# Performance work log

Measured on AMD Instinct MI355X. Metric: run time of the kernel, lower is better.

## Reference

```python
import jax, jax.numpy as jnp
import numpy as np

B, N, T, D = 2, 4, 512, 1024
DK, H, E = 64, 8, 6
D_ATTN = 512
DV = D_ATTN // H            # 64
DKP = 2 * DK                # PoPE doubles key dim -> 128
HE = H * E                  # 48
R = max(DK // 4, 1)         # LoRA rank 16
DA = int(DK * 1.618)        # 103
CC = D_ATTN                 # concat dim 512
DPG = max(int(CC * 0.618), 1)  # 316
ND = N * D
ROUTE_TEMP = 1.0


def _sinkhorn(M, n_iters=6):
    M = jnp.exp(M)
    for _ in range(n_iters):
        M = M / jnp.sum(M, -1, keepdims=True)
        M = M / jnp.sum(M, -2, keepdims=True)
    return M


def _pope(x, phi):
    mu = jax.nn.softplus(x)
    return jnp.concatenate([mu * jnp.cos(phi), mu * jnp.sin(phi)], -1)


def setup_inputs():
    ks = iter(jax.random.split(jax.random.key(0), 24))
    def rn(s, sc=0.01):
        return jax.random.normal(next(ks), s, jnp.float32) * sc
    return {
        'stream': jax.random.normal(next(ks), (B, N, T, D), jnp.float32),
        'freqs': 10000.0 ** (jnp.arange(DK, dtype=jnp.float32) / DK),
        'pope_delta_raw': jnp.zeros((DK,), jnp.float32),
        'W_q_w': rn((H, DK, D)), 'W_k_w': rn((H, DK, D)), 'W_v_w': rn((H, DV, D)),
        'q_router_w': rn((H, E, D), 0.02), 'kv_router_w': rn((H, E, D), 0.02),
        'lora_A_q': rn((HE, D, R)), 'lora_B_q': jnp.zeros((HE, R, DK), jnp.float32),
        'lora_A_k': rn((HE, D, R)), 'lora_B_k': jnp.zeros((HE, R, DK), jnp.float32),
        'lora_A_v': rn((HE, D, R)), 'lora_B_v': jnp.zeros((HE, R, DV), jnp.float32),
        'alpha_up_w': rn((HE, D, DA)), 'alpha_down_w': rn((HE, DA, DKP)),
        'beta_up_w': rn((HE, D, DA)), 'beta_down_w': rn((HE, DA, 1)),
        'mhc_norm_w': jnp.ones((HE, ND), jnp.float32),
        'phi_pre_w': rn((HE, N, ND)), 'phi_post_w': rn((HE, N, ND)),
        'phi_res_w': rn((HE, N * N, ND)),
        'b_pre': jnp.zeros((HE, N), jnp.float32), 'b_post': jnp.zeros((HE, N), jnp.float32),
        'b_res': jnp.zeros((HE, N, N), jnp.float32),
        'alpha_pre': jnp.ones((HE,), jnp.float32), 'alpha_post': jnp.ones((HE,), jnp.float32),
        'alpha_res': jnp.ones((HE,), jnp.float32),
        'batched_norm_w': jnp.ones((HE, D), jnp.float32),
        'W_pre_w': rn((HE, D, CC)), 'W_o_w': rn((D, CC)),
        'W_pg1_w': rn((HE, D, DPG)), 'W_pg2_w': rn((HE, DPG, D)),
    }


def reference(stream, freqs, pope_delta_raw, W_q_w, W_k_w, W_v_w, q_router_w, kv_router_w,
              lora_A_q, lora_B_q, lora_A_k, lora_B_k, lora_A_v, lora_B_v,
              alpha_up_w, alpha_down_w, beta_up_w, beta_down_w,
              mhc_norm_w, phi_pre_w, phi_post_w, phi_res_w, b_pre, b_post, b_res,
              alpha_pre, alpha_post, alpha_res, batched_norm_w,
              W_pre_w, W_o_w, W_pg1_w, W_pg2_w):
    positions = jnp.arange(T, dtype=jnp.float32)
    # ---- per-head top-1 routing (eval-mode argmax, straight-through probs) ----
    route_in = jnp.mean(stream, axis=1)                                # (B,T,D)
    q_logits = jnp.clip(jnp.einsum('btd,hed->hbte', route_in, q_router_w), -10, 10)
    kv_logits = jnp.clip(jnp.einsum('btd,hed->hbte', route_in, kv_router_w), -10, 10)
    q_probs = jax.nn.softmax(q_logits / ROUTE_TEMP, -1)
    kv_probs = jax.nn.softmax(kv_logits / ROUTE_TEMP, -1)
    q_oh = jax.nn.one_hot(jnp.argmax(q_logits, -1), E, dtype=stream.dtype)
    kv_oh = jax.nn.one_hot(jnp.argmax(kv_logits, -1), E, dtype=stream.dtype)
    eff_q = q_probs + jax.lax.stop_gradient(q_oh - q_probs)            # (H,B,T,E)
    eff_kv = kv_probs + jax.lax.stop_gradient(kv_oh - kv_probs)
    eff_q = eff_q.transpose(0, 3, 1, 2).reshape(HE, B, T)              # h-major, k=h*E+e
    eff_kv = eff_kv.transpose(0, 3, 1, 2).reshape(HE, B, T)
    # ---- batched MHC over all HE experts (dense form of active-set gather) ----
    x = stream.transpose(0, 2, 1, 3).reshape(B, T, ND)
    x = x * jax.lax.rsqrt(jnp.mean(jnp.square(x), -1, keepdims=True) + 1e-8)
    H_pre = jax.nn.sigmoid(alpha_pre[:, None, None, None] *
                           jnp.einsum('btd,knd->kbtn', x, phi_pre_w * mhc_norm_w[:, None, :])
                           + b_pre[:, None, None, :])
    H_post = 2 * jax.nn.sigmoid(alpha_post[:, None, None, None] *
                                jnp.einsum('btd,knd->kbtn', x, phi_post_w * mhc_norm_w[:, None, :])
                                + b_post[:, None, None, :])
    res = jnp.einsum('btd,knd->kbtn', x, phi_res_w * mhc_norm_w[:, None, :]).reshape(HE, B, T, N, N)
    H_res = _sinkhorn(alpha_res[:, None, None, None, None] * res + b_res[:, None, None, :, :])
    h_e = jnp.einsum('kbtn,bntd->kbtd', H_pre, stream)                 # (HE,B,T,D)
    h_e = h_e * jax.lax.rsqrt(jnp.mean(jnp.square(h_e), -1, keepdims=True) + 1e-8) * batched_norm_w[:, None, None, :]
    # ---- expert q/k/v with LoRA + PoPE ----
    phi = positions[:, None] * freqs[None, :]                          # (T,DK)
    phi_k = phi - 2 * jnp.pi * jax.nn.sigmoid(pope_delta_raw)[None, :]
    Wq = jnp.repeat(W_q_w, E, 0); Wk = jnp.repeat(W_k_w, E, 0); Wv = jnp.repeat(W_v_w, E, 0)
    def lora(h, A, Bm):
        return jnp.einsum('kbtr,kro->kbto', jax.nn.silu(jnp.einsum('kbtd,kdr->kbtr', h, A)), Bm)
    def l2n(v):
        return v * jax.lax.rsqrt(jnp.sum(jnp.square(v), -1, keepdims=True) + 1e-12)
    q_p = l2n(jnp.einsum('kbtd,kod->kbto', h_e, Wq) + lora(h_e, lora_A_q, lora_B_q))
    k_p = l2n(jnp.einsum('kbtd,kod->kbto', h_e, Wk) + lora(h_e, lora_A_k, lora_B_k))
    v_p = jnp.einsum('kbtd,kod->kbto', h_e, Wv) + lora(h_e, lora_A_v, lora_B_v)
    qmask = (jnp.arange(HE) % E > 0).astype(stream.dtype)[:, None, None, None]  # expert 0 = no-op for Q
    q_out = _pope(q_p, phi[None, None]) * qmask                        # (HE,B,T,DKP)
    k_out = _pope(k_p, phi_k[None, None])
    a_out = jax.nn.sigmoid(jnp.einsum('kbta,kap->kbtp', jax.nn.silu(jnp.einsum('kbtd,kda->kbta', h_e, alpha_up_w)), alpha_down_w))
    b_out = jax.nn.sigmoid(jnp.einsum('kbta,kap->kbtp', jax.nn.silu(jnp.einsum('kbtd,kda->kbta', h_e, beta_up_w)), beta_down_w))
    def mix(w, vals):
        return (w[..., None] * vals).reshape(H, E, B, T, vals.shape[-1]).sum(1)  # (H,B,T,*)
    q_buf = mix(eff_q, q_out); k_buf = mix(eff_kv, k_out); v_buf = mix(eff_kv, v_p)
    a_buf = mix(eff_kv, a_out); b_buf = mix(eff_kv, b_out)
    # ---- KDA delta-rule state recursion via lax.scan over time ----
    def step(S, xs):
        q_t, k_t, v_t, a_t, b_t = xs                                   # (H,B,dim)
        aS = a_t[..., None] * S                                        # (H,B,DKP,DV)
        ktaS = jnp.einsum('hbd,hbde->hbe', k_t, aS)
        S = aS + b_t[..., None] * (k_t[..., None] * (v_t - ktaS)[..., None, :])
        return S, jnp.einsum('hbd,hbde->hbe', q_t, S)
    tf = lambda z: jnp.moveaxis(z, 2, 0)                               # (T,H,B,*)
    S0 = jnp.zeros((H, B, DKP, DV), stream.dtype)
    _, outs = jax.lax.scan(step, S0, (tf(q_buf), tf(k_buf), tf(v_buf), tf(a_buf), tf(b_buf)))
    attn = outs.transpose(2, 0, 1, 3).reshape(B, T, H * DV)            # concat heads
    # ---- gates, output projection, MHC write-back ----
    pre_gate = jax.nn.sigmoid(jnp.einsum('kbt,kbtd,kdc->btc', eff_kv, h_e, W_pre_w))
    pg = jax.nn.silu(jnp.einsum('kbtd,kdp->kbtp', h_e, W_pg1_w))
    post_gate = jax.nn.sigmoid(jnp.einsum('kbt,kbtp,kpd->btd', eff_kv, pg, W_pg2_w))
    y = jnp.einsum('btc,dc->btd', attn * pre_gate, W_o_w) * post_gate
    Hres_acc = jnp.einsum('kbt,kbtnm->btnm', eff_kv, H_res) / H
    Hpost_acc = jnp.einsum('kbt,kbtn->btn', eff_kv, H_post) / H
    return jnp.einsum('btnm,bmtd->bntd', Hres_acc, stream) + jnp.einsum('btn,btd->bntd', Hpost_acc, y)
```

## Files before the change

### kernel.cpp

```cpp
#include <hip/hip_runtime.h>
#include <math.h>

#define DEV static __device__ __forceinline__

#define B_   2
#define N_   4
#define T_   512
#define D_   1024
#define DK_  64
#define H_   8
#define E_   6
#define DV_  64
#define DKP_ 128
#define HE_  48
#define R_   16
#define DA_  103
#define CC_  512
#define DPG_ 316
#define ND_  4096
#define U_   1024

typedef unsigned short u16;
typedef __attribute__((ext_vector_type(8))) unsigned short us8;
typedef __attribute__((ext_vector_type(8))) short bhalf8;
typedef __attribute__((ext_vector_type(4))) float f32x4;

struct P {
  const float *stream, *freqs, *pope_delta;
  const float *W_q, *W_k, *W_v, *q_rw, *kv_rw;
  const float *lA_q, *lB_q, *lA_k, *lB_k, *lA_v, *lB_v;
  const float *a_up, *a_dn, *b_up, *b_dn;
  const float *mhc_norm, *phi_pre, *phi_post, *phi_res;
  const float *b_pre, *b_post, *b_res, *al_pre, *al_post, *al_res;
  const float *bn_w, *W_pre, *W_o, *W_pg1, *W_pg2;
  int *qsel, *kvsel, *qcnt, *kvcnt, *qlist, *kvlist;
  float *scale, *mhc_partial;
  float *Hpre_q, *Hpre_kv, *Hres, *Hpost;
  float *kv_lin, *aup, *bup, *pre_logit, *post_logit;
  float *la_k, *la_v, *la_q, *q_lin;
  float *a_buf, *b_buf, *q_buf, *k_buf, *v_buf;
  float *attn, *y;
  float *out;
  u16 *xb;
  u16 *he_kvB, *he_qB, *pgB;
  u16 *Bt0, *Bt1, *Bt2, *Bt3, *Bt4;
};

DEV float sigm(float x){ return 1.f/(1.f+expf(-x)); }
DEV float softplus_(float x){ return x>0.f ? x+log1pf(expf(-x)) : log1pf(expf(x)); }
DEV float silu_(float x){ return x*sigm(x); }
DEV u16 f2b(float x){ unsigned u = __float_as_uint(x); u += 0x7FFFu + ((u>>16)&1u); return (u16)(u>>16); }

DEV float block_reduce_sum(float v, float* sm){
  __syncthreads();
  int lane = threadIdx.x & 63, w = threadIdx.x >> 6;
  for (int off=32; off; off>>=1) v += __shfl_down(v, off, 64);
  if (lane==0) sm[w] = v;
  __syncthreads();
  if (threadIdx.x == 0){
    float s = 0; int nw = blockDim.x >> 6;
    for (int i=0;i<nw;i++) s += sm[i];
    sm[0] = s;
  }
  __syncthreads();
  return sm[0];
}


__global__ void k_prep0(P p){
  int j = blockIdx.x; int k = j/24, r = j%24;
  const float* src;
  if (r < 4)      src = p.phi_pre  + (size_t)(k*4+r)*ND_;
  else if (r < 8) src = p.phi_post + (size_t)(k*4+(r-4))*ND_;
  else            src = p.phi_res  + (size_t)(k*16+(r-8))*ND_;
  const float* mn = p.mhc_norm + (size_t)k*ND_;
  u16* d = p.Bt0 + (size_t)j*ND_;
  for (int i = threadIdx.x; i < ND_; i += 256) d[i] = f2b(src[i]*mn[i]);
}

__global__ void k_prep1d(P p){
  int r = blockIdx.x, g = blockIdx.y, h = g/E_;
  u16* drow = p.Bt1 + (size_t)g*1216*1024 + (size_t)(r<128 ? r : 1194 + (r-128))*1024;
  const float* srow = (r<64) ? (p.W_k + ((size_t)h*64 + r)*1024)
                   : (r<128) ? (p.W_v + ((size_t)h*64 + (r-64))*1024) : nullptr;
  for (int k2 = threadIdx.x; k2 < 1024; k2 += 256)
    drow[k2] = (r<128) ? f2b(srow[k2]) : (u16)0;
}

__global__ void k_prep2d(P p){
  int r = blockIdx.x, g = blockIdx.y, h = g/E_;
  u16* drow = p.Bt2 + (size_t)g*128*1024 + (size_t)r*1024;
  const float* srow = p.W_q + ((size_t)h*64 + r)*1024;
  for (int k2 = threadIdx.x; k2 < 1024; k2 += 256) drow[k2] = f2b(srow[k2]);
}

__global__ void k_prep4(P p){
  int r = blockIdx.x;
  u16* drow = p.Bt4 + (size_t)r*512;
  const float* srow = p.W_o + (size_t)r*512;
  for (int c = threadIdx.x; c < 512; c += 256) drow[c] = f2b(srow[c]);
}

__global__ void k_prept(const float* src, long sstride, int ld, int ncols,
                        u16* dst, long dstride, int dld, int K, int Ksrc){
  __shared__ float t[32][33];
  const float* S = src + (size_t)blockIdx.z*sstride;
  u16* Dp = dst + (size_t)blockIdx.z*dstride;
  int k0 = blockIdx.x*32, c0 = blockIdx.y*32;
  int tx = threadIdx.x & 31, ty = threadIdx.x >> 5;
  #pragma unroll
  for (int i=0;i<32;i+=8){
    int k = k0+ty+i, c = c0+tx;
    t[ty+i][tx] = (k < Ksrc && c < ncols) ? S[(size_t)k*ld + c] : 0.f;
  }
  __syncthreads();
  #pragma unroll
  for (int i=0;i<32;i+=8){
    int c = c0+ty+i, k = k0+tx;
    if (c < ncols && k < K) Dp[(size_t)c*dld + k] = f2b(t[tx][ty+i]);
  }
}


__global__ void k_route(P p){
  int u = blockIdx.x, b = u>>9, t = u&511;
  __shared__ float ri[D_];
  __shared__ float lg[2][HE_];
  __shared__ float sm[8];
  int tid = threadIdx.x;
  float sv[4][4]; float ss = 0.f;
  #pragma unroll
  for (int j=0;j<4;j++){
    int d = tid + j*256;
    float acc = 0;
    #pragma unroll
    for (int n = 0; n < 4; n++){
      float v = p.stream[(((size_t)(b*N_+n)*T_)+t)*D_ + d];
      sv[j][n] = v; acc += v; ss += v*v;
    }
    ri[d] = acc * 0.25f;
  }
  ss = block_reduce_sum(ss, sm);
  float sc = rsqrtf(ss/(float)ND_ + 1e-8f);
  if (tid==0) p.scale[u] = sc;
  #pragma unroll
  for (int j=0;j<4;j++){
    int d = tid + j*256;
    #pragma unroll
    for (int n=0;n<4;n++)
      p.xb[(size_t)u*ND_ + n*D_ + d] = f2b(sv[j][n]*sc);
  }
  int lane = tid & 63, wv = tid >> 6;
  for (int j = wv; j < 2*HE_; j += 4){
    const float* w = (j < HE_ ? p.q_rw : p.kv_rw) + (size_t)(j % HE_)*D_;
    float acc = 0;
    for (int d = lane; d < D_; d += 64) acc += ri[d]*w[d];
    for (int off=32; off; off>>=1) acc += __shfl_down(acc, off, 64);
    if (lane==0) lg[j/HE_][j%HE_] = acc;
  }
  __syncthreads();
  if (tid < 16){
    int h = tid & 7, which = tid >> 3;
    const float* L = lg[which] + h*E_;
    float best = fminf(fmaxf(L[0],-10.f),10.f); int bi=0;
    for (int e=1;e<E_;e++){ float v=fminf(fmaxf(L[e],-10.f),10.f); if (v>best){best=v;bi=e;} }
    int g = h*E_+bi;
    if (which==0){ p.qsel[h*U_+u]=bi;  int pos=atomicAdd(&p.qcnt[g],1);  p.qlist[g*U_+pos]=u; }
    else         { p.kvsel[h*U_+u]=bi; int pos=atomicAdd(&p.kvcnt[g],1); p.kvlist[g*U_+pos]=u; }
  }
}


template<int MODE>
__global__ __launch_bounds__(256) void k_mgemm(P p){
  const int n0 = blockIdx.x * 128;
  const int m0 = blockIdx.y * 128;
  const int g  = blockIdx.z;
  const int h  = g / E_;
  int K, NO, cnt;
  const int* list = nullptr;
  const u16* Bsrc;
  if (MODE==0){ K=1024; NO=1152; cnt=U_; Bsrc=p.Bt0; }
  else if (MODE==1){ K=1024; NO=1194; cnt=p.kvcnt[g]; list=p.kvlist+g*U_; Bsrc=p.Bt1+(size_t)g*1216*1024; }
  else if (MODE==2){ K=1024; NO=80;   cnt=p.qcnt[g];  list=p.qlist +g*U_; Bsrc=p.Bt2+(size_t)g*128*1024; }
  else if (MODE==3){ K=320;  NO=1024; cnt=p.kvcnt[g]; list=p.kvlist+g*U_; Bsrc=p.Bt3+(size_t)g*1024*320; }
  else { K=512; NO=1024; cnt=U_; Bsrc=p.Bt4; }
  if (m0 >= cnt) return;
  const int rows = min(128, cnt - m0);

  __shared__ u16 Asl[128*32];
  __shared__ u16 Bsl[128*32];
  __shared__ int toks[128];
  const int tid = threadIdx.x;
  if (tid < 128){
    if (MODE==0||MODE==4) toks[tid] = m0 + tid;
    else toks[tid] = (tid < rows) ? list[m0+tid] : list[m0];
  }
  __syncthreads();

  f32x4 acc[4][4];
  #pragma unroll
  for (int i=0;i<4;i++)
    #pragma unroll
    for (int j=0;j<4;j++) acc[i][j] = (f32x4)(0.f);

  const int lane = tid & 63, wv = tid >> 6;
  const int wr = (wv>>1)*64, wc = (wv&1)*64;
  const int l16 = lane & 15, kce = lane >> 4;

  for (int k0 = 0; k0 < K; k0 += 32){
    #pragma unroll
    for (int pass=0; pass<2; pass++){
      int m = (tid>>2) + pass*64;
      int kc4 = tid & 3;
      int ks = k0 + kc4*8;
      us8 av;
      if (MODE==1){
        int u = toks[m];
        av = *(const us8*)&p.he_kvB[((size_t)(h*U_+u))*1024 + ks];
      } else if (MODE==2){
        int u = toks[m];
        av = *(const us8*)&p.he_qB[((size_t)(h*U_+u))*1024 + ks];
      } else if (MODE==3){
        int u = toks[m];
        av = *(const us8*)&p.pgB[((size_t)(h*U_+u))*320 + ks];
      } else if (MODE==0){
        int u = toks[m];
        av = *(const us8*)&p.xb[(size_t)u*ND_ + g*1024 + ks];
      } else {
        int u = toks[m];
        const float* ap = p.attn + (size_t)u*CC_ + ks;
        const float* pp = p.pre_logit + (size_t)u*CC_ + ks;
        float4 a0 = *(const float4*)ap, a1 = *(const float4*)(ap+4);
        float4 q0 = *(const float4*)pp, q1 = *(const float4*)(pp+4);
        av[0]=f2b(a0.x*sigm(q0.x)); av[1]=f2b(a0.y*sigm(q0.y));
        av[2]=f2b(a0.z*sigm(q0.z)); av[3]=f2b(a0.w*sigm(q0.w));
        av[4]=f2b(a1.x*sigm(q1.x)); av[5]=f2b(a1.y*sigm(q1.y));
        av[6]=f2b(a1.z*sigm(q1.z)); av[7]=f2b(a1.w*sigm(q1.w));
      }
      *(us8*)&Asl[m*32 + kc4*8] = av;
    }
    #pragma unroll
    for (int pass=0; pass<2; pass++){
      int n = (tid>>2) + pass*64;
      int kc4 = tid & 3;
      int ks = k0 + kc4*8;
      int gn = n0 + n;
      us8 bv = (us8)((u16)0);
      if (MODE==1){ if (gn < 1216) bv = *(const us8*)&Bsrc[(size_t)gn*1024 + ks]; }
      else if (MODE==0){ bv = *(const us8*)&Bsrc[(size_t)gn*4096 + g*1024 + ks]; }
      else if (MODE==2){ bv = *(const us8*)&Bsrc[(size_t)gn*1024 + ks]; }
      else if (MODE==3){ bv = *(const us8*)&Bsrc[(size_t)gn*320 + ks]; }
      else { bv = *(const us8*)&Bsrc[(size_t)gn*512 + ks]; }
      *(us8*)&Bsl[n*32 + kc4*8] = bv;
    }
    __syncthreads();
    bhalf8 af[4], bf4[4];
    #pragma unroll
    for (int i=0;i<4;i++) af[i] = *(const bhalf8*)&Asl[(wr + i*16 + l16)*32 + kce*8];
    #pragma unroll
    for (int j=0;j<4;j++) bf4[j] = *(const bhalf8*)&Bsl[(wc + j*16 + l16)*32 + kce*8];
    #pragma unroll
    for (int i=0;i<4;i++)
      #pragma unroll
      for (int j=0;j<4;j++)
        acc[i][j] = __builtin_amdgcn_mfma_f32_16x16x32_bf16(af[i], bf4[j], acc[i][j], 0, 0, 0);
    __syncthreads();
  }

  #pragma unroll
  for (int i=0;i<4;i++){
    #pragma unroll
    for (int r=0;r<4;r++){
      int rl = wr + i*16 + kce*4 + r;
      if (rl >= rows) continue;
      int u = toks[rl];
      #pragma unroll
      for (int j=0;j<4;j++){
        int cg = n0 + wc + j*16 + l16;
        if (cg >= NO) continue;
        float v = acc[i][j][r];
        if (MODE==0){
          p.mhc_partial[(size_t)g*U_*1152 + (size_t)u*1152 + cg] = v;
        } else if (MODE==1){
          size_t base = (size_t)(h*U_+u);
          if (cg < 128)       p.kv_lin[base*128 + cg] = v;
          else if (cg < 231)  p.aup[base*DA_ + (cg-128)] = silu_(v);
          else if (cg < 334)  p.bup[base*DA_ + (cg-231)] = silu_(v);
          else if (cg < 846)  atomicAdd(&p.pre_logit[(size_t)u*CC_ + (cg-334)], v);
          else if (cg < 1162) p.pgB[base*320 + (cg-846)] = f2b(silu_(v));
          else if (cg < 1178) p.la_k[base*R_ + (cg-1162)] = silu_(v);
          else                p.la_v[base*R_ + (cg-1178)] = silu_(v);
        } else if (MODE==2){
          size_t base = (size_t)(h*U_+u);
          if (cg < 64) p.q_lin[base*64 + cg] = v;
          else         p.la_q[base*R_ + (cg-64)] = silu_(v);
        } else if (MODE==3){
          atomicAdd(&p.post_logit[(size_t)u*D_ + cg], v);
        } else {
          p.y[(size_t)u*D_ + cg] = v * sigm(p.post_logit[(size_t)u*D_ + cg]);
        }
      }
    }
  }
}


DEV float lgread(const float* Pp, int j){
  const size_t S = (size_t)U_*1152;
  return Pp[j] + Pp[j+S] + Pp[j+2*S] + Pp[j+3*S];
}

__global__ void k_mhcsel(P p){
  int u = blockIdx.x;
  int tid = threadIdx.x;
  __shared__ float racc[8][16];
  __shared__ float pacc[8][4];
  if (tid < 8){
    int h = tid;
    const float* lg = p.mhc_partial + (size_t)u*1152;
    int kq = h*E_ + p.qsel[h*U_+u];
    for (int n=0;n<4;n++)
      p.Hpre_q[(size_t)(h*U_+u)*4 + n] = sigm(p.al_pre[kq]*lgread(lg,kq*24+n) + p.b_pre[kq*4+n]);
    int kk = h*E_ + p.kvsel[h*U_+u];
    for (int n=0;n<4;n++)
      p.Hpre_kv[(size_t)(h*U_+u)*4 + n] = sigm(p.al_pre[kk]*lgread(lg,kk*24+n) + p.b_pre[kk*4+n]);
    for (int n=0;n<4;n++)
      pacc[h][n] = 2.f*sigm(p.al_post[kk]*lgread(lg,kk*24+4+n) + p.b_post[kk*4+n]);
    float M[4][4];
    for (int n=0;n<4;n++)
      for (int m=0;m<4;m++)
        M[n][m] = expf(p.al_res[kk]*lgread(lg,kk*24+8+n*4+m) + p.b_res[kk*16+n*4+m]);
    for (int it=0; it<6; it++){
      for (int n=0;n<4;n++){ float s=M[n][0]+M[n][1]+M[n][2]+M[n][3]; float r=1.f/s;
        for(int m=0;m<4;m++) M[n][m]*=r; }
      for (int m=0;m<4;m++){ float s=M[0][m]+M[1][m]+M[2][m]+M[3][m]; float r=1.f/s;
        for(int n=0;n<4;n++) M[n][m]*=r; }
    }
    for (int n=0;n<4;n++) for (int m=0;m<4;m++) racc[h][n*4+m] = M[n][m];
  }
  __syncthreads();
  if (tid < 16){
    float s=0; for (int h=0;h<8;h++) s += racc[h][tid];
    p.Hres[(size_t)u*16 + tid] = s * 0.125f;
  }
  if (tid < 4){
    float s=0; for (int h=0;h<8;h++) s += pacc[h][tid];
    p.Hpost[(size_t)u*4 + tid] = s * 0.125f;
  }
}

__global__ void k_he(P p){
  int id = blockIdx.x;
  int path = id >> 13;
  int h = (id >> 10) & 7;
  int u = id & 1023;
  int b = u>>9, t = u&511;
  int sel = path ? p.kvsel[h*U_+u] : p.qsel[h*U_+u];
  int k = h*E_ + sel;
  const float* Hp = (path ? p.Hpre_kv : p.Hpre_q) + (size_t)(h*U_+u)*4;
  float w0=Hp[0], w1=Hp[1], w2=Hp[2], w3=Hp[3];
  float v[4];
  float ss = 0;
  int tid = threadIdx.x;
  #pragma unroll
  for (int j=0;j<4;j++){
    int d = tid + j*256;
    float s0 = p.stream[(((size_t)(b*N_+0)*T_)+t)*D_ + d];
    float s1 = p.stream[(((size_t)(b*N_+1)*T_)+t)*D_ + d];
    float s2 = p.stream[(((size_t)(b*N_+2)*T_)+t)*D_ + d];
    float s3 = p.stream[(((size_t)(b*N_+3)*T_)+t)*D_ + d];
    v[j] = w0*s0 + w1*s1 + w2*s2 + w3*s3;
    ss += v[j]*v[j];
  }
  __shared__ float sm[8];
  ss = block_reduce_sum(ss, sm);
  float sc = rsqrtf(ss/(float)D_ + 1e-8f);
  u16* out = (path ? p.he_kvB : p.he_qB) + (size_t)(h*U_+u)*D_;
  #pragma unroll
  for (int j=0;j<4;j++){
    int d = tid + j*256;
    out[d] = f2b(v[j]*sc*p.bn_w[(size_t)k*D_ + d]);
  }
}

__global__ void k_stage2(P p){
  int id = blockIdx.x;
  int h = id >> 10, u = id & 1023;
  int t = u & 511;
  int kkv = h*E_ + p.kvsel[h*U_+u];
  size_t base = (size_t)(h*U_+u);
  __shared__ float s_au[DA_], s_bu[DA_], s_lk[R_], s_lv[R_], s_lq[R_], s_kl[64], s_vl[64], s_ql[64];
  int tid = threadIdx.x;
  if (tid < DA_){ s_au[tid] = p.aup[base*DA_+tid]; s_bu[tid] = p.bup[base*DA_+tid]; }
  if (tid < R_){ s_lk[tid] = p.la_k[base*R_+tid]; s_lv[tid] = p.la_v[base*R_+tid]; s_lq[tid] = p.la_q[base*R_+tid]; }
  if (tid >= 64 && tid < 128){
    s_kl[tid-64] = p.kv_lin[base*128 + (tid-64)];
    s_vl[tid-64] = p.kv_lin[base*128 + 64 + (tid-64)];
  }
  if (tid < 64) s_ql[tid] = p.q_lin[base*64 + tid];
  __syncthreads();
  {
    float acc = 0;
    const float* W = p.a_dn + (size_t)kkv*DA_*DKP_;
    for (int a=0;a<DA_;a++) acc += s_au[a]*W[a*DKP_ + tid];
    p.a_buf[base*DKP_ + tid] = sigm(acc);
  }
  if (tid == 0){
    float acc = 0;
    const float* W = p.b_dn + (size_t)kkv*DA_;
    for (int a=0;a<DA_;a++) acc += s_bu[a]*W[a];
    p.b_buf[base] = sigm(acc);
  }
  if (tid < 64){
    int o = tid;
    float lbk=0.f, lbv=0.f;
    for (int r=0;r<R_;r++){
      lbk += s_lk[r]*p.lB_k[((size_t)kkv*R_+r)*DK_ + o];
      lbv += s_lv[r]*p.lB_v[((size_t)kkv*R_+r)*DV_ + o];
    }
    float kl = s_kl[o] + lbk;
    float ss = kl*kl;
    for (int off=1; off<64; off<<=1) ss += __shfl_xor(ss, off, 64);
    float kp = kl * rsqrtf(ss + 1e-12f);
    float mu = softplus_(kp);
    float ph = (float)t * p.freqs[o] - 6.2831855f * sigm(p.pope_delta[o]);
    p.k_buf[base*DKP_ + o]      = mu * cosf(ph);
    p.k_buf[base*DKP_ + 64 + o] = mu * sinf(ph);
    p.v_buf[base*DV_ + o] = s_vl[o] + lbv;
  } else {
    int o = tid - 64;
    int sel = p.qsel[h*U_+u];
    if (sel == 0){
      p.q_buf[base*DKP_ + o] = 0.f;
      p.q_buf[base*DKP_ + 64 + o] = 0.f;
    } else {
      int kq = h*E_ + sel;
      float lbq = 0.f;
      for (int r=0;r<R_;r++) lbq += s_lq[r]*p.lB_q[((size_t)kq*R_+r)*DK_+o];
      float ql = s_ql[o] + lbq;
      float ss = ql*ql;
      for (int off=1; off<64; off<<=1) ss += __shfl_xor(ss, off, 64);
      float qp = ql*rsqrtf(ss + 1e-12f);
      float mu = softplus_(qp);
      float ph = (float)t * p.freqs[o];
      p.q_buf[base*DKP_ + o]      = mu*cosf(ph);
      p.q_buf[base*DKP_ + 64 + o] = mu*sinf(ph);
    }
  }
}

__global__ __launch_bounds__(256) void k_scan(P p){
  const int h = blockIdx.x >> 1, b = blockIdx.x & 1;
  const int tid = threadIdx.x;
  const int e = tid & 63;
  const int qd = __builtin_amdgcn_readfirstlane(tid >> 6);
  const int d0 = qd * 32;
  const size_t hb = (size_t)(h*U_ + b*T_);
  float s[32];
  #pragma unroll
  for (int i=0;i<32;i++) s[i]=0.f;
  __shared__ float sq[2][128];
  __shared__ float part[2][4][64];
  __shared__ float part2[4][64];
  float rq = (tid<128) ? p.q_buf[hb*128 + tid] : 0.f;
  if (tid<128) sq[0][tid] = rq;
  rq = (tid<128) ? p.q_buf[(hb+1)*128 + tid] : 0.f;
  __syncthreads();
  for (int t=0;t<T_;t++){
    const int bb = t&1;
    const size_t base = hb + t;
    const float* kp = p.k_buf + base*128 + d0;
    const float* ap = p.a_buf + base*128 + d0;
    float kr[32], ar[32];
    #pragma unroll
    for (int i=0;i<32;i++){ kr[i]=kp[i]; ar[i]=ap[i]; }
    float bs = p.b_buf[base];
    float vv = p.v_buf[base*64 + e];
    float pa = 0.f;
    #pragma unroll
    for (int i=0;i<32;i++) pa += (ar[i]*s[i])*kr[i];
    part[bb][qd][e] = pa;
    __syncthreads();
    float w = vv - (part[bb][0][e]+part[bb][1][e]+part[bb][2][e]+part[bb][3][e]);
    float bw = bs * w;
    float o = 0.f;
    #pragma unroll
    for (int i=0;i<32;i++){
      s[i] = ar[i]*s[i] + bw*kr[i];
      o += sq[bb][d0+i] * s[i];
    }
    if (tid < 128) sq[bb^1][tid] = rq;
    part2[qd][e] = o;
    __syncthreads();
    if (tid < 64){
      float r = part2[0][tid]+part2[1][tid]+part2[2][tid]+part2[3][tid];
      p.attn[(size_t)(b*T_+t)*CC_ + h*64 + tid] = r;
    }
    if (tid < 128 && t+2 < T_) rq = p.q_buf[(hb+t+2)*128 + tid];
  }
}

__global__ void k_final(P p){
  int u = blockIdx.x, b=u>>9, t=u&511;
  __shared__ float hr[16], hp[4];
  if (threadIdx.x < 16) hr[threadIdx.x] = p.Hres[(size_t)u*16+threadIdx.x];
  if (threadIdx.x < 4)  hp[threadIdx.x] = p.Hpost[(size_t)u*4+threadIdx.x];
  __syncthreads();
  for (int d = threadIdx.x; d < D_; d += 256){
    float yv = p.y[(size_t)u*D_ + d];
    float sm0 = p.stream[(((size_t)(b*N_+0)*T_)+t)*D_ + d];
    float sm1 = p.stream[(((size_t)(b*N_+1)*T_)+t)*D_ + d];
    float sm2 = p.stream[(((size_t)(b*N_+2)*T_)+t)*D_ + d];
    float sm3 = p.stream[(((size_t)(b*N_+3)*T_)+t)*D_ + d];
    #pragma unroll
    for (int n=0;n<4;n++){
      float v = hr[n*4+0]*sm0 + hr[n*4+1]*sm1 + hr[n*4+2]*sm2 + hr[n*4+3]*sm3 + hp[n]*yv;
      p.out[(((size_t)(b*N_+n)*T_)+t)*D_ + d] = v;
    }
  }
}


extern "C" void kernel_launch(void* const* d_in, const int* in_sizes, int n_in,
                              void* d_out, int out_size, void* d_ws, size_t ws_size,
                              hipStream_t stream){
  P p;
  p.stream = (const float*)d_in[0];
  p.freqs = (const float*)d_in[1];
  p.pope_delta = (const float*)d_in[2];
  p.W_q = (const float*)d_in[3]; p.W_k = (const float*)d_in[4]; p.W_v = (const float*)d_in[5];
  p.q_rw = (const float*)d_in[6]; p.kv_rw = (const float*)d_in[7];
  p.lA_q = (const float*)d_in[8];  p.lB_q = (const float*)d_in[9];
  p.lA_k = (const float*)d_in[10]; p.lB_k = (const float*)d_in[11];
  p.lA_v = (const float*)d_in[12]; p.lB_v = (const float*)d_in[13];
  p.a_up = (const float*)d_in[14]; p.a_dn = (const float*)d_in[15];
  p.b_up = (const float*)d_in[16]; p.b_dn = (const float*)d_in[17];
  p.mhc_norm = (const float*)d_in[18];
  p.phi_pre = (const float*)d_in[19]; p.phi_post = (const float*)d_in[20]; p.phi_res = (const float*)d_in[21];
  p.b_pre = (const float*)d_in[22]; p.b_post = (const float*)d_in[23]; p.b_res = (const float*)d_in[24];
  p.al_pre = (const float*)d_in[25]; p.al_post = (const float*)d_in[26]; p.al_res = (const float*)d_in[27];
  p.bn_w = (const float*)d_in[28];
  p.W_pre = (const float*)d_in[29]; p.W_o = (const float*)d_in[30];
  p.W_pg1 = (const float*)d_in[31]; p.W_pg2 = (const float*)d_in[32];
  p.out = (float*)d_out;

  char* w = (char*)d_ws;
  size_t off = 0;
  auto alloc = [&](size_t bytes)->void*{
    void* r = w + off;
    off = (off + bytes + 255) & ~(size_t)255;
    return r;
  };
  p.qsel   = (int*)alloc(H_*U_*4);
  p.kvsel  = (int*)alloc(H_*U_*4);
  p.qcnt   = (int*)alloc(HE_*4);
  p.kvcnt  = (int*)alloc(HE_*4);
  p.qlist  = (int*)alloc((size_t)HE_*U_*4);
  p.kvlist = (int*)alloc((size_t)HE_*U_*4);
  p.scale  = (float*)alloc(U_*4);
  p.mhc_partial = (float*)alloc((size_t)4*U_*1152*4);
  p.Hpre_q  = (float*)alloc((size_t)H_*U_*4*4);
  p.Hpre_kv = (float*)alloc((size_t)H_*U_*4*4);
  p.Hres    = (float*)alloc((size_t)U_*16*4);
  p.Hpost   = (float*)alloc((size_t)U_*4*4);
  p.kv_lin  = (float*)alloc((size_t)H_*U_*128*4);
  p.aup     = (float*)alloc((size_t)H_*U_*DA_*4);
  p.bup     = (float*)alloc((size_t)H_*U_*DA_*4);
  p.pre_logit  = (float*)alloc((size_t)U_*CC_*4);
  p.post_logit = (float*)alloc((size_t)U_*D_*4);
  p.la_k    = (float*)alloc((size_t)H_*U_*R_*4);
  p.la_v    = (float*)alloc((size_t)H_*U_*R_*4);
  p.la_q    = (float*)alloc((size_t)H_*U_*R_*4);
  p.q_lin   = (float*)alloc((size_t)H_*U_*64*4);
  p.a_buf   = (float*)alloc((size_t)H_*U_*DKP_*4);
  p.b_buf   = (float*)alloc((size_t)H_*U_*4);
  p.q_buf   = (float*)alloc((size_t)H_*U_*DKP_*4);
  p.k_buf   = (float*)alloc((size_t)H_*U_*DKP_*4);
  p.v_buf   = (float*)alloc((size_t)H_*U_*DV_*4);
  p.attn    = (float*)alloc((size_t)U_*CC_*4);
  p.y       = (float*)alloc((size_t)U_*D_*4);
  p.xb      = (u16*)alloc((size_t)U_*ND_*2);
  p.he_kvB = (u16*)alloc((size_t)H_*U_*D_*2);
  p.he_qB  = (u16*)alloc((size_t)H_*U_*D_*2);
  p.pgB    = (u16*)alloc((size_t)H_*U_*320*2);
  p.Bt0    = (u16*)alloc((size_t)1152*4096*2);
  p.Bt1    = (u16*)alloc((size_t)HE_*1216*1024*2);
  p.Bt2    = (u16*)alloc((size_t)HE_*128*1024*2);
  p.Bt3    = (u16*)alloc((size_t)HE_*1024*320*2);
  p.Bt4    = (u16*)alloc((size_t)1024*512*2);
  if (off > ws_size) return;

  hipMemsetAsync(p.qcnt, 0, HE_*4, stream);
  hipMemsetAsync(p.kvcnt, 0, HE_*4, stream);
  hipMemsetAsync(p.pre_logit, 0, (size_t)U_*CC_*4, stream);
  hipMemsetAsync(p.post_logit, 0, (size_t)U_*D_*4, stream);
  hipMemsetAsync(p.pgB, 0, (size_t)H_*U_*320*2, stream);
  hipMemsetAsync(p.Bt2, 0, (size_t)HE_*128*1024*2, stream);

  k_prep0<<<1152,256,0,stream>>>(p);
  k_prep1d<<<dim3(150,48),256,0,stream>>>(p);
  size_t b1s = (size_t)1216*1024;
  k_prept<<<dim3(32, 4,48),256,0,stream>>>(p.a_up,  (long)1024*DA_, DA_, DA_, p.Bt1+ 128*1024, b1s, 1024, 1024, 1024);
  k_prept<<<dim3(32, 4,48),256,0,stream>>>(p.b_up,  (long)1024*DA_, DA_, DA_, p.Bt1+ 231*1024, b1s, 1024, 1024, 1024);
  k_prept<<<dim3(32,16,48),256,0,stream>>>(p.W_pre, (long)1024*CC_, CC_, CC_, p.Bt1+ 334*1024, b1s, 1024, 1024, 1024);
  k_prept<<<dim3(32,10,48),256,0,stream>>>(p.W_pg1, (long)1024*DPG_,DPG_,DPG_,p.Bt1+ 846*1024, b1s, 1024, 1024, 1024);
  k_prept<<<dim3(32, 1,48),256,0,stream>>>(p.lA_k,  (long)1024*R_,  R_,  R_,  p.Bt1+1162*1024, b1s, 1024, 1024, 1024);
  k_prept<<<dim3(32, 1,48),256,0,stream>>>(p.lA_v,  (long)1024*R_,  R_,  R_,  p.Bt1+1178*1024, b1s, 1024, 1024, 1024);
  k_prep2d<<<dim3(64,48),256,0,stream>>>(p);
  k_prept<<<dim3(32, 1,48),256,0,stream>>>(p.lA_q,  (long)1024*R_,  R_,  R_,  p.Bt2+  64*1024, (long)128*1024, 1024, 1024, 1024);
  k_prept<<<dim3(10,32,48),256,0,stream>>>(p.W_pg2, (long)DPG_*1024,1024,1024,p.Bt3,           (long)1024*320,  320,  320,  316);
  k_prep4<<<1024,256,0,stream>>>(p);

  k_route<<<U_,256,0,stream>>>(p);
  k_mgemm<0><<<dim3(9,8,4),256,0,stream>>>(p);
  k_mhcsel<<<U_,64,0,stream>>>(p);
  k_he<<<2*H_*U_,256,0,stream>>>(p);
  k_mgemm<1><<<dim3(10,8,48),256,0,stream>>>(p);
  k_mgemm<2><<<dim3(1,8,48),256,0,stream>>>(p);
  k_stage2<<<H_*U_,128,0,stream>>>(p);
  k_mgemm<3><<<dim3(8,8,48),256,0,stream>>>(p);
  k_scan<<<16,256,0,stream>>>(p);
  k_mgemm<4><<<dim3(8,8,1),256,0,stream>>>(p);
  k_final<<<U_,256,0,stream>>>(p);
}
```

Before: 1.622 ms.

## Split scan into single-wave blocks with DPP reductions; merge he kernel per token

The recurrent scan moves from 16 blocks of 256 threads, which needed two barriers per timestep, to 64 single-wavefront blocks. Each block owns 16 value columns, and each group of 4 lanes splits the key dimension, with cross-lane DPP quad reductions replacing the shared-memory partial sums and barriers. Key, decay and query loads are double-buffered one step ahead. Separately, the he-normalization kernel now handles all 16 head/path combinations per token in one block, so the four stream rows are loaded once instead of 16 times. The costs are higher register pressure in both kernels and a scan where each thread recomputes per-column work.

New measurement: 1.540 ms. 5.1% less time.

```diff
diff --git a/kernel.cpp b/kernel.cpp
--- a/kernel.cpp
+++ b/kernel.cpp
@@ -50,6 +50,11 @@
 DEV float softplus_(float x){ return x>0.f ? x+log1pf(expf(-x)) : log1pf(expf(x)); }
 DEV float silu_(float x){ return x*sigm(x); }
 DEV u16 f2b(float x){ unsigned u = __float_as_uint(x); u += 0x7FFFu + ((u>>16)&1u); return (u16)(u>>16); }
+
+template<int CTRL>
+DEV float dppq(float x){
+  return __int_as_float(__builtin_amdgcn_mov_dpp(__float_as_int(x), CTRL, 0xF, 0xF, true));
+}
 
 DEV float block_reduce_sum(float v, float* sm){
   __syncthreads();
@@ -350,37 +355,68 @@
   }
 }
 
-__global__ void k_he(P p){
-  int id = blockIdx.x;
-  int path = id >> 13;
-  int h = (id >> 10) & 7;
-  int u = id & 1023;
-  int b = u>>9, t = u&511;
-  int sel = path ? p.kvsel[h*U_+u] : p.qsel[h*U_+u];
-  int k = h*E_ + sel;
-  const float* Hp = (path ? p.Hpre_kv : p.Hpre_q) + (size_t)(h*U_+u)*4;
-  float w0=Hp[0], w1=Hp[1], w2=Hp[2], w3=Hp[3];
-  float v[4];
-  float ss = 0;
+__global__ __launch_bounds__(256) void k_he2(P p){
+  int u = blockIdx.x, b = u>>9, t = u&511;
   int tid = threadIdx.x;
+  int lane = tid & 63, wv = tid >> 6;
+  __shared__ float wts[16][4];
+  __shared__ int   ksl[16];
+  __shared__ float red[16][4];
+  __shared__ float scl[16];
+  if (tid < 16){
+    int path = tid >> 3, h = tid & 7;
+    int sel = path ? p.kvsel[h*U_+u] : p.qsel[h*U_+u];
+    ksl[tid] = h*E_ + sel;
+    const float* Hp = (path ? p.Hpre_kv : p.Hpre_q) + (size_t)(h*U_+u)*4;
+    #pragma unroll
+    for (int n=0;n<4;n++) wts[tid][n] = Hp[n];
+  }
+  __syncthreads();
+  float s[4][4];
   #pragma unroll
   for (int j=0;j<4;j++){
     int d = tid + j*256;
-    float s0 = p.stream[(((size_t)(b*N_+0)*T_)+t)*D_ + d];
-    float s1 = p.stream[(((size_t)(b*N_+1)*T_)+t)*D_ + d];
-    float s2 = p.stream[(((size_t)(b*N_+2)*T_)+t)*D_ + d];
-    float s3 = p.stream[(((size_t)(b*N_+3)*T_)+t)*D_ + d];
-    v[j] = w0*s0 + w1*s1 + w2*s2 + w3*s3;
-    ss += v[j]*v[j];
-  }
-  __shared__ float sm[8];
-  ss = block_reduce_sum(ss, sm);
-  float sc = rsqrtf(ss/(float)D_ + 1e-8f);
-  u16* out = (path ? p.he_kvB : p.he_qB) + (size_t)(h*U_+u)*D_;
-  #pragma unroll
-  for (int j=0;j<4;j++){
-    int d = tid + j*256;
-    out[d] = f2b(v[j]*sc*p.bn_w[(size_t)k*D_ + d]);
+    #pragma unroll
+    for (int n=0;n<4;n++)
+      s[j][n] = p.stream[(((size_t)(b*N_+n)*T_)+t)*D_ + d];
+  }
+  float ssl[16];
+  #pragma unroll
+  for (int c=0;c<16;c++){
+    float w0=wts[c][0], w1=wts[c][1], w2=wts[c][2], w3=wts[c][3];
+    float acc = 0;
+    #pragma unroll
+    for (int j=0;j<4;j++){
+      float v = w0*s[j][0] + w1*s[j][1] + w2*s[j][2] + w3*s[j][3];
+      acc += v*v;
+    }
+    ssl[c] = acc;
+  }
+  #pragma unroll
+  for (int c=0;c<16;c++){
+    float v = ssl[c];
+    for (int off=32; off; off>>=1) v += __shfl_down(v, off, 64);
+    if (lane==0) red[c][wv] = v;
+  }
+  __syncthreads();
+  if (tid < 16){
+    float ssum = red[tid][0]+red[tid][1]+red[tid][2]+red[tid][3];
+    scl[tid] = rsqrtf(ssum/(float)D_ + 1e-8f);
+  }
+  __syncthreads();
+  #pragma unroll
+  for (int c=0;c<16;c++){
+    float w0=wts[c][0], w1=wts[c][1], w2=wts[c][2], w3=wts[c][3];
+    float sc = scl[c];
+    int k = ksl[c];
+    int h = c & 7;
+    u16* out = (c>=8 ? p.he_kvB : p.he_qB) + (size_t)(h*U_+u)*D_;
+    #pragma unroll
+    for (int j=0;j<4;j++){
+      int d = tid + j*256;
+      float v = w0*s[j][0] + w1*s[j][1] + w2*s[j][2] + w3*s[j][3];
+      out[d] = f2b(v*sc*p.bn_w[(size_t)k*D_ + d]);
+    }
   }
 }
 
@@ -450,54 +486,56 @@
   }
 }
 
-__global__ __launch_bounds__(256) void k_scan(P p){
-  const int h = blockIdx.x >> 1, b = blockIdx.x & 1;
-  const int tid = threadIdx.x;
-  const int e = tid & 63;
-  const int qd = __builtin_amdgcn_readfirstlane(tid >> 6);
-  const int d0 = qd * 32;
+#define LOADSET(kR,aR,qR,vR,bR,tt) {                                      \
+  int tc=(tt); size_t bb = hb + tc;                                       \
+  const float4* kp_=(const float4*)(p.k_buf+bb*128+d0);                   \
+  const float4* ap_=(const float4*)(p.a_buf+bb*128+d0);                   \
+  const float4* qp_=(const float4*)(p.q_buf+bb*128+d0);                   \
+  _Pragma("unroll") for(int i_=0;i_<8;i_++){ kR[i_]=kp_[i_]; aR[i_]=ap_[i_]; qR[i_]=qp_[i_]; } \
+  vR = p.v_buf[bb*64+e]; bR = p.b_buf[bb]; }
+
+#define STEPSET(kR,aR,qR,vR,bR,tt) {                                      \
+  float p0=0,p1=0,p2=0,p3=0;                                              \
+  _Pragma("unroll") for(int i_=0;i_<8;i_++){                              \
+    float4 sv=s4[i_]; float4 av=aR[i_]; float4 kv=kR[i_];                 \
+    sv.x*=av.x; sv.y*=av.y; sv.z*=av.z; sv.w*=av.w;                       \
+    p0+=kv.x*sv.x; p1+=kv.y*sv.y; p2+=kv.z*sv.z; p3+=kv.w*sv.w;           \
+    s4[i_]=sv; }                                                          \
+  float pt=(p0+p1)+(p2+p3);                                               \
+  pt += dppq<0xB1>(pt); pt += dppq<0x4E>(pt);                             \
+  float bw = bR*(vR-pt);                                                  \
+  float o0=0,o1=0,o2=0,o3=0;                                              \
+  _Pragma("unroll") for(int i_=0;i_<8;i_++){                              \
+    float4 sv=s4[i_]; float4 kv=kR[i_]; float4 qv=qR[i_];                 \
+    sv.x+=bw*kv.x; sv.y+=bw*kv.y; sv.z+=bw*kv.z; sv.w+=bw*kv.w;           \
+    o0+=qv.x*sv.x; o1+=qv.y*sv.y; o2+=qv.z*sv.z; o3+=qv.w*sv.w;           \
+    s4[i_]=sv; }                                                          \
+  float ot=(o0+o1)+(o2+o3);                                               \
+  ot += dppq<0xB1>(ot); ot += dppq<0x4E>(ot);                             \
+  if (dg==0) p.attn[(size_t)(b*T_+(tt))*CC_ + h*64 + e] = ot; }
+
+__global__ __launch_bounds__(64, 1) void k_scan(P p){
+  const int h  = blockIdx.x >> 3;
+  const int b  = (blockIdx.x >> 2) & 1;
+  const int ec = blockIdx.x & 3;
+  const int lane = threadIdx.x;
+  const int dg = lane & 3;
+  const int el = lane >> 2;
+  const int e  = ec*16 + el;
+  const int d0 = dg*32;
   const size_t hb = (size_t)(h*U_ + b*T_);
-  float s[32];
-  #pragma unroll
-  for (int i=0;i<32;i++) s[i]=0.f;
-  __shared__ float sq[2][128];
-  __shared__ float part[2][4][64];
-  __shared__ float part2[4][64];
-  float rq = (tid<128) ? p.q_buf[hb*128 + tid] : 0.f;
-  if (tid<128) sq[0][tid] = rq;
-  rq = (tid<128) ? p.q_buf[(hb+1)*128 + tid] : 0.f;
-  __syncthreads();
-  for (int t=0;t<T_;t++){
-    const int bb = t&1;
-    const size_t base = hb + t;
-    const float* kp = p.k_buf + base*128 + d0;
-    const float* ap = p.a_buf + base*128 + d0;
-    float kr[32], ar[32];
-    #pragma unroll
-    for (int i=0;i<32;i++){ kr[i]=kp[i]; ar[i]=ap[i]; }
-    float bs = p.b_buf[base];
-    float vv = p.v_buf[base*64 + e];
-    float pa = 0.f;
-    #pragma unroll
-    for (int i=0;i<32;i++) pa += (ar[i]*s[i])*kr[i];
-    part[bb][qd][e] = pa;
-    __syncthreads();
-    float w = vv - (part[bb][0][e]+part[bb][1][e]+part[bb][2][e]+part[bb][3][e]);
-    float bw = bs * w;
-    float o = 0.f;
-    #pragma unroll
-    for (int i=0;i<32;i++){
-      s[i] = ar[i]*s[i] + bw*kr[i];
-      o += sq[bb][d0+i] * s[i];
-    }
-    if (tid < 128) sq[bb^1][tid] = rq;
-    part2[qd][e] = o;
-    __syncthreads();
-    if (tid < 64){
-      float r = part2[0][tid]+part2[1][tid]+part2[2][tid]+part2[3][tid];
-      p.attn[(size_t)(b*T_+t)*CC_ + h*64 + tid] = r;
-    }
-    if (tid < 128 && t+2 < T_) rq = p.q_buf[(hb+t+2)*128 + tid];
+  float4 s4[8];
+  #pragma unroll
+  for (int i=0;i<8;i++) s4[i] = make_float4(0.f,0.f,0.f,0.f);
+  float4 kA[8], aA[8], qA[8], kB[8], aB[8], qB[8];
+  float vA, bA, vB, bB;
+  LOADSET(kA,aA,qA,vA,bA, 0);
+  LOADSET(kB,aB,qB,vB,bB, 1);
+  for (int t=0;t<T_;t+=2){
+    STEPSET(kA,aA,qA,vA,bA, t);
+    LOADSET(kA,aA,qA,vA,bA, (t+2<T_)? t+2 : T_-1);
+    STEPSET(kB,aB,qB,vB,bB, t+1);
+    LOADSET(kB,aB,qB,vB,bB, (t+3<T_)? t+3 : T_-1);
   }
 }
 
@@ -615,12 +653,12 @@
   k_route<<<U_,256,0,stream>>>(p);
   k_mgemm<0><<<dim3(9,8,4),256,0,stream>>>(p);
   k_mhcsel<<<U_,64,0,stream>>>(p);
-  k_he<<<2*H_*U_,256,0,stream>>>(p);
+  k_he2<<<U_,256,0,stream>>>(p);
   k_mgemm<1><<<dim3(10,8,48),256,0,stream>>>(p);
   k_mgemm<2><<<dim3(1,8,48),256,0,stream>>>(p);
   k_stage2<<<H_*U_,128,0,stream>>>(p);
   k_mgemm<3><<<dim3(8,8,48),256,0,stream>>>(p);
-  k_scan<<<16,256,0,stream>>>(p);
+  k_scan<<<64,64,0,stream>>>(p);
   k_mgemm<4><<<dim3(8,8,1),256,0,stream>>>(p);
   k_final<<<U_,256,0,stream>>>(p);
 }
```
